# Kernel tuning notes

Measured on AMD Instinct MI355X. Metric: run time of the kernel, lower is better.

The kernel has to match this reference:

```python
import jax, jax.numpy as jnp
import numpy as np

H = 16  # num_heads
D = 1024  # hidden_dim
HD = D // H  # head_dim


def setup_inputs() -> dict:
    key = jax.random.key(0)
    ks = jax.random.split(key, 12)
    B, S = 2, 2048
    x = jax.random.normal(ks[0], (B, S, D), dtype=jnp.float32)
    attention_bias = jax.random.normal(ks[1], (H, S, S), dtype=jnp.float32) * 0.1
    # padding mask: True = masked; last (S - len) positions padded, no all-masked rows
    lengths = jax.random.randint(ks[2], (B,), S // 2, S + 1)
    key_padding_mask = jnp.arange(S)[None, :] >= lengths[:, None]  # [B, S] bool
    s = 1.0 / np.sqrt(D)
    Wq = jax.random.normal(ks[3], (D, D), dtype=jnp.float32) * s
    bq = jnp.zeros((D,), dtype=jnp.float32)
    Wk = jax.random.normal(ks[4], (D, D), dtype=jnp.float32) * s
    bk = jnp.zeros((D,), dtype=jnp.float32)
    Wv = jax.random.normal(ks[5], (D, D), dtype=jnp.float32) * s
    bv = jnp.zeros((D,), dtype=jnp.float32)
    Wo = jax.random.normal(ks[6], (D, D), dtype=jnp.float32) * s
    bo = jnp.zeros((D,), dtype=jnp.float32)
    return {"x": x, "attention_bias": attention_bias, "key_padding_mask": key_padding_mask,
            "Wq": Wq, "bq": bq, "Wk": Wk, "bk": bk, "Wv": Wv, "bv": bv, "Wo": Wo, "bo": bo}


def reference(x, attention_bias, key_padding_mask, Wq, bq, Wk, bk, Wv, bv, Wo, bo):
    B, S, _ = x.shape
    scale = HD ** (-0.5)

    def shape_heads(t):  # [B,S,D] -> [B,H,S,HD]
        return t.reshape(B, S, H, HD).transpose(0, 2, 1, 3)

    q = shape_heads(x @ Wq + bq)
    k = shape_heads(x @ Wk + bk)
    v = shape_heads(x @ Wv + bv)

    attn = jnp.einsum('bhqd,bhkd->bhqk', q, k) * scale  # [B,H,S,S]
    attn = attn + attention_bias[None]
    attn = jnp.where(key_padding_mask[:, None, None, :], -jnp.inf, attn)

    # handle fully-masked rows: zero their logits pre-softmax, zero weights after
    all_masked = jnp.all(key_padding_mask, axis=1)  # [B]
    bad = all_masked[:, None, None, None]
    safe_attn = jnp.where(bad, 0.0, attn)
    weights = jax.nn.softmax(safe_attn, axis=-1)
    weights = jnp.where(bad, 0.0, weights)

    context = jnp.einsum('bhqk,bhkd->bhqd', weights, v)  # [B,H,S,HD]
    context = context.transpose(0, 2, 1, 3).reshape(B, S, D)
    return context @ Wo + bo
```

## Files before the change

kernel.cpp:

```cpp
#include <hip/hip_runtime.h>
#include <hip/hip_bf16.h>
#include <stdint.h>

#define BB 2
#define SS 2048
#define DDIM 1024
#define HH 16
#define HDIM 64

typedef __hip_bfloat16 bf16;
typedef __bf16 bf16x8 __attribute__((ext_vector_type(8)));
typedef float f32x4 __attribute__((ext_vector_type(4)));
typedef short short8 __attribute__((ext_vector_type(8)));
typedef short s16x4 __attribute__((ext_vector_type(4)));

static __device__ __forceinline__ f32x4 mfma16(bf16x8 a, bf16x8 b, f32x4 c) {
  return __builtin_amdgcn_mfma_f32_16x16x32_bf16(a, b, c, 0, 0, 0);
}

static __device__ __forceinline__ void gload_lds16(const void* g, void* l) {
  __builtin_amdgcn_global_load_lds(
      (const __attribute__((address_space(1))) void*)g,
      (__attribute__((address_space(3))) void*)l, 16, 0, 0);
}

__global__ __launch_bounds__(256) void cvt_k(const float* __restrict__ src,
                                             bf16* __restrict__ dst) {
  const int base = (blockIdx.x * 256 + threadIdx.x) * 8;
  float4 a = *reinterpret_cast<const float4*>(src + base);
  float4 b = *reinterpret_cast<const float4*>(src + base + 4);
  union {
    bf16 h[8];
    short8 v;
  } u;
  u.h[0] = __float2bfloat16(a.x);
  u.h[1] = __float2bfloat16(a.y);
  u.h[2] = __float2bfloat16(a.z);
  u.h[3] = __float2bfloat16(a.w);
  u.h[4] = __float2bfloat16(b.x);
  u.h[5] = __float2bfloat16(b.y);
  u.h[6] = __float2bfloat16(b.z);
  u.h[7] = __float2bfloat16(b.w);
  *reinterpret_cast<short8*>(dst + base) = u.v;
}

__global__ __launch_bounds__(256) void transpose_cvt_k(
    const float* __restrict__ src, bf16* __restrict__ dst) {
  __shared__ float tile[64][65];
  const int t = threadIdx.x;
  const int r = t >> 2, c0 = (t & 3) * 16;
  const int bx = blockIdx.x * 64, by = blockIdx.y * 64;
  const float* sp = src + (size_t)(by + r) * DDIM + bx + c0;
#pragma unroll
  for (int j = 0; j < 16; ++j) tile[r][c0 + j] = sp[j];
  __syncthreads();
  bf16* dp = dst + (size_t)(bx + r) * DDIM + by + c0;
#pragma unroll
  for (int j = 0; j < 16; ++j) dp[j] = __float2bfloat16(tile[c0 + j][r]);
}

__global__ __launch_bounds__(64) void mask_pack_k(
    const int* __restrict__ kpm, unsigned long long* __restrict__ mb) {
  const int i = threadIdx.x;
  const int b = i >> 5, c = i & 31;
  unsigned long long bits = 0ull;
  for (int j = 0; j < 64; ++j)
    bits |= (unsigned long long)(kpm[b * SS + c * 64 + j] != 0) << j;
  mb[i] = bits;
}

template <int MODE>
__global__ __launch_bounds__(256, 2) void gemm_bt(
    const bf16* __restrict__ A, const bf16* __restrict__ Bt,
    const float* __restrict__ b0, const float* __restrict__ b1,
    const float* __restrict__ b2, bf16* __restrict__ O0,
    bf16* __restrict__ O1, bf16* __restrict__ O2, float* __restrict__ Of) {
  constexpr int Kd = DDIM;
  __shared__ bf16x8 lA[128 * 8];
  __shared__ bf16x8 lB[128 * 8];
  const int tid = threadIdx.x;
  const int wave = tid >> 6, lane = tid & 63;
  const int l15 = lane & 15, l4 = lane >> 4;
  const int wm = wave >> 1, wn = wave & 1;
  const int m0 = blockIdx.x * 128, n0 = blockIdx.y * 128;
  const f32x4 z = {0.f, 0.f, 0.f, 0.f};
  f32x4 acc[4][4];
#pragma unroll
  for (int i = 0; i < 4; ++i)
#pragma unroll
    for (int j = 0; j < 4; ++j) acc[i][j] = z;

  for (int k0 = 0; k0 < Kd; k0 += 64) {
#pragma unroll
    for (int j = 0; j < 4; ++j) {
      const int slot = j * 256 + tid;
      const int r = slot >> 3, cs = slot & 7;
      const int c = cs ^ (r & 7);
      gload_lds16(A + (size_t)(m0 + r) * Kd + k0 + c * 8,
                  &lA[j * 256 + wave * 64]);
      gload_lds16(Bt + (size_t)(n0 + r) * Kd + k0 + c * 8,
                  &lB[j * 256 + wave * 64]);
    }
    __syncthreads();
    bf16x8 af[2][4], bfr[2][4];
#pragma unroll
    for (int ks = 0; ks < 2; ++ks) {
#pragma unroll
      for (int i = 0; i < 4; ++i) {
        const int ra = wm * 64 + i * 16 + l15;
        af[ks][i] = lA[ra * 8 + ((ks * 4 + l4) ^ (ra & 7))];
        const int rb = wn * 64 + i * 16 + l15;
        bfr[ks][i] = lB[rb * 8 + ((ks * 4 + l4) ^ (rb & 7))];
      }
    }
#pragma unroll
    for (int ks = 0; ks < 2; ++ks)
#pragma unroll
      for (int i = 0; i < 4; ++i)
#pragma unroll
        for (int j = 0; j < 4; ++j)
          acc[i][j] = mfma16(af[ks][i], bfr[ks][j], acc[i][j]);
    __syncthreads();
  }

#pragma unroll
  for (int i = 0; i < 4; ++i) {
    const int m = m0 + wm * 64 + i * 16 + l4 * 4;
#pragma unroll
    for (int j = 0; j < 4; ++j) {
      const int n = n0 + wn * 64 + j * 16 + l15;
      if (MODE == 1) {
        const float bb = b0[n];
#pragma unroll
        for (int r = 0; r < 4; ++r)
          Of[(size_t)(m + r) * DDIM + n] = acc[i][j][r] + bb;
      } else {
        const int sel = n >> 10, nn = n & 1023;
        const int h = nn >> 6, d = nn & 63;
        const float* bp = sel == 0 ? b0 : (sel == 1 ? b1 : b2);
        const float bb = bp[nn];
        const int b = m >> 11, s = m & 2047;
        if (sel == 2) {
          union {
            bf16 h4[4];
            s16x4 v;
          } u;
#pragma unroll
          for (int r = 0; r < 4; ++r)
            u.h4[r] = __float2bfloat16(acc[i][j][r] + bb);
          *reinterpret_cast<s16x4*>(
              &O2[((size_t)(b * HH + h) * HDIM + d) * SS + s]) = u.v;
        } else {
#pragma unroll
          for (int r = 0; r < 4; ++r) {
            const float val = acc[i][j][r] + bb;
            (sel ? O1 : O0)[((size_t)(b * HH + h) * SS + (s + r)) * HDIM + d] =
                __float2bfloat16(val);
          }
        }
      }
    }
  }
}

__global__ __launch_bounds__(256, 2) void attn_k(
    const bf16* __restrict__ Qb, const bf16* __restrict__ Kb,
    const bf16* __restrict__ Vt, const float* __restrict__ bias,
    const unsigned long long* __restrict__ mbits, bf16* __restrict__ ctx) {
  __shared__ bf16x8 lK[2][512];
  __shared__ bf16x8 lV[2][512];
  __shared__ f32x4 lB[2][1024];
  __shared__ unsigned int plP[4 * 512];
  const int tid = threadIdx.x;
  const int wave = tid >> 6, lane = tid & 63;
  const int l15 = lane & 15, l4 = lane >> 4;
  const int bid = blockIdx.x;
  const int qblk = bid & 31, bh = bid >> 5;
  const int b = bh >> 4, h = bh & 15;
  const int q0b = qblk * 64;
  const int q0w = q0b + wave * 16;

  const bf16* Qp = Qb + ((size_t)bh * SS + q0w) * HDIM;
  const bf16* Kp = Kb + (size_t)bh * SS * HDIM;
  const bf16* Vp = Vt + (size_t)bh * HDIM * SS;
  const float* Bb = bias + (size_t)h * SS * SS + (size_t)q0b * SS;
  unsigned int* plw = plP + wave * 512;

  const int rk0 = tid >> 3, ck0 = tid & 7;
  const int rk1 = 32 + rk0, ck1 = ck0;
  const int dk0 = rk0 * 8 + (ck0 ^ (rk0 & 7));
  const int dk1 = rk1 * 8 + (ck1 ^ (rk1 & 7));
  int rbv[4], cbv[4], dbv[4];
#pragma unroll
  for (int i = 0; i < 4; ++i) {
    const int sb = i * 256 + tid;
    rbv[i] = sb >> 4;
    cbv[i] = sb & 15;
    dbv[i] = rbv[i] * 16 + (cbv[i] ^ (rbv[i] & 7));
  }
  const int brow = wave * 16 + l15;

  {
    bf16x8 k0 = *reinterpret_cast<const bf16x8*>(Kp + (size_t)rk0 * HDIM + ck0 * 8);
    bf16x8 k1 = *reinterpret_cast<const bf16x8*>(Kp + (size_t)rk1 * HDIM + ck1 * 8);
    bf16x8 v0 = *reinterpret_cast<const bf16x8*>(Vp + (size_t)rk0 * SS + ck0 * 8);
    bf16x8 v1 = *reinterpret_cast<const bf16x8*>(Vp + (size_t)rk1 * SS + ck1 * 8);
    f32x4 b0 = *reinterpret_cast<const f32x4*>(Bb + (size_t)rbv[0] * SS + cbv[0] * 4);
    f32x4 b1 = *reinterpret_cast<const f32x4*>(Bb + (size_t)rbv[1] * SS + cbv[1] * 4);
    f32x4 b2 = *reinterpret_cast<const f32x4*>(Bb + (size_t)rbv[2] * SS + cbv[2] * 4);
    f32x4 b3 = *reinterpret_cast<const f32x4*>(Bb + (size_t)rbv[3] * SS + cbv[3] * 4);
    lK[0][dk0] = k0;
    lK[0][dk1] = k1;
    lV[0][dk0] = v0;
    lV[0][dk1] = v1;
    lB[0][dbv[0]] = b0;
    lB[0][dbv[1]] = b1;
    lB[0][dbv[2]] = b2;
    lB[0][dbv[3]] = b3;
  }

  bf16x8 qf[2];
#pragma unroll
  for (int ks = 0; ks < 2; ++ks)
    qf[ks] = *reinterpret_cast<const bf16x8*>(Qp + (size_t)l15 * HDIM +
                                              ks * 32 + l4 * 8);
  const f32x4 z = {0.f, 0.f, 0.f, 0.f};
  f32x4 o[4];
#pragma unroll
  for (int dd = 0; dd < 4; ++dd) o[dd] = z;
  float mrow = -1e30f, lrow = 0.f;

  __syncthreads();

  for (int t = 0; t < 32; ++t) {
    const int cur = t & 1;
    const int kbn = (t + 1) * 64;
    const bool pf = t < 31;

    bf16x8 ks0, ks1, vs0, vs1;
    f32x4 bs0, bs1, bs2, bs3;
    if (pf) {
      ks0 = *reinterpret_cast<const bf16x8*>(Kp + (size_t)(kbn + rk0) * HDIM + ck0 * 8);
      ks1 = *reinterpret_cast<const bf16x8*>(Kp + (size_t)(kbn + rk1) * HDIM + ck1 * 8);
      vs0 = *reinterpret_cast<const bf16x8*>(Vp + (size_t)rk0 * SS + kbn + ck0 * 8);
      vs1 = *reinterpret_cast<const bf16x8*>(Vp + (size_t)rk1 * SS + kbn + ck1 * 8);
      bs0 = *reinterpret_cast<const f32x4*>(Bb + (size_t)rbv[0] * SS + kbn + cbv[0] * 4);
      bs1 = *reinterpret_cast<const f32x4*>(Bb + (size_t)rbv[1] * SS + kbn + cbv[1] * 4);
      bs2 = *reinterpret_cast<const f32x4*>(Bb + (size_t)rbv[2] * SS + kbn + cbv[2] * 4);
      bs3 = *reinterpret_cast<const f32x4*>(Bb + (size_t)rbv[3] * SS + kbn + cbv[3] * 4);
    }

    f32x4 sc[4];
#pragma unroll
    for (int jj = 0; jj < 4; ++jj) {
      const int R = jj * 16 + l15;
      bf16x8 kf0 = lK[cur][R * 8 + ((0 + l4) ^ (R & 7))];
      bf16x8 kf1 = lK[cur][R * 8 + ((4 + l4) ^ (R & 7))];
      f32x4 s = mfma16(kf0, qf[0], z);
      s = mfma16(kf1, qf[1], s);
      sc[jj] = s;
    }
    const unsigned long long mb = mbits[(b << 5) + t];
    float v[4][4];
    float bm = -1e30f;
#pragma unroll
    for (int jj = 0; jj < 4; ++jj) {
      const int byte =
          brow * 256 + ((((jj * 4 + l4) ^ (l15 & 7))) * 16);
      const f32x4 b4 = *reinterpret_cast<const f32x4*>(
          reinterpret_cast<const char*>(&lB[cur][0]) + byte);
      const unsigned nib = (unsigned)(mb >> (jj * 16 + l4 * 4)) & 15u;
#pragma unroll
      for (int r = 0; r < 4; ++r) {
        const float a = ((nib >> r) & 1u) ? -1e30f : b4[r];
        v[jj][r] = fmaf(sc[jj][r], 0.125f, a);
        bm = fmaxf(bm, v[jj][r]);
      }
    }
    bm = fmaxf(bm, __shfl_xor(bm, 16));
    bm = fmaxf(bm, __shfl_xor(bm, 32));
    const float mn = fmaxf(mrow, bm);
    const float alpha = __expf(mrow - mn);
    mrow = mn;
    float ps = 0.f;
    float p[4][4];
#pragma unroll
    for (int jj = 0; jj < 4; ++jj)
#pragma unroll
      for (int r = 0; r < 4; ++r) {
        p[jj][r] = __expf(v[jj][r] - mn);
        ps += p[jj][r];
      }
    ps += __shfl_xor(ps, 16);
    ps += __shfl_xor(ps, 32);
    lrow = lrow * alpha + ps;
#pragma unroll
    for (int jj = 0; jj < 4; ++jj)
#pragma unroll
      for (int r0 = 0; r0 < 4; r0 += 2) {
        union {
          bf16 h2[2];
          unsigned int w;
        } u;
        u.h2[0] = __float2bfloat16(p[jj][r0]);
        u.h2[1] = __float2bfloat16(p[jj][r0 + 1]);
        const int byte =
            (l15 * 128 + jj * 32 + l4 * 8 + r0 * 2) ^ ((l15 & 7) << 4);
        plw[byte >> 2] = u.w;
      }
    asm volatile("s_waitcnt lgkmcnt(0)" ::: "memory");
    bf16x8 pfr[2];
#pragma unroll
    for (int ks = 0; ks < 2; ++ks) {
      const int byte = (l15 * 128 + ks * 64 + l4 * 16) ^ ((l15 & 7) << 4);
      pfr[ks] = *reinterpret_cast<const bf16x8*>(
          reinterpret_cast<const char*>(plw) + byte);
    }
    float ar[4];
#pragma unroll
    for (int r = 0; r < 4; ++r) ar[r] = __shfl(alpha, l4 * 4 + r);
#pragma unroll
    for (int dd = 0; dd < 4; ++dd) {
      const int D = dd * 16 + l15;
      bf16x8 vf0 = lV[cur][D * 8 + ((0 + l4) ^ (D & 7))];
      bf16x8 vf1 = lV[cur][D * 8 + ((4 + l4) ^ (D & 7))];
#pragma unroll
      for (int r = 0; r < 4; ++r) o[dd][r] *= ar[r];
      o[dd] = mfma16(pfr[0], vf0, o[dd]);
      o[dd] = mfma16(pfr[1], vf1, o[dd]);
    }

    if (pf) {
      const int nxt = cur ^ 1;
      lK[nxt][dk0] = ks0;
      lK[nxt][dk1] = ks1;
      lV[nxt][dk0] = vs0;
      lV[nxt][dk1] = vs1;
      lB[nxt][dbv[0]] = bs0;
      lB[nxt][dbv[1]] = bs1;
      lB[nxt][dbv[2]] = bs2;
      lB[nxt][dbv[3]] = bs3;
    }
    __syncthreads();
  }

  const float rl = 1.0f / lrow;
  float rlr[4];
#pragma unroll
  for (int r = 0; r < 4; ++r) rlr[r] = __shfl(rl, l4 * 4 + r);
#pragma unroll
  for (int dd = 0; dd < 4; ++dd) {
#pragma unroll
    for (int r = 0; r < 4; ++r) {
      const float val = o[dd][r] * rlr[r];
      const int s = q0w + l4 * 4 + r;
      ctx[((size_t)b * SS + s) * DDIM + h * HDIM + dd * 16 + l15] =
          __float2bfloat16(val);
    }
  }
}

extern "C" void kernel_launch(void* const* d_in, const int* in_sizes, int n_in,
                              void* d_out, int out_size, void* d_ws,
                              size_t ws_size, hipStream_t stream) {
  const float* x = (const float*)d_in[0];
  const float* abias = (const float*)d_in[1];
  const int* kpm = (const int*)d_in[2];
  const float* Wq = (const float*)d_in[3];
  const float* bq = (const float*)d_in[4];
  const float* Wk = (const float*)d_in[5];
  const float* bk = (const float*)d_in[6];
  const float* Wv = (const float*)d_in[7];
  const float* bv = (const float*)d_in[8];
  const float* Wo = (const float*)d_in[9];
  const float* bo = (const float*)d_in[10];
  float* out = (float*)d_out;

  char* ws = (char*)d_ws;
  bf16* xb = (bf16*)ws;
  bf16* Wt = (bf16*)(ws + 8388608);
  bf16* Wot = (bf16*)(ws + 14680064);
  bf16* Qb = (bf16*)(ws + 16777216);
  bf16* Kb = (bf16*)(ws + 25165824);
  bf16* Vtb = (bf16*)(ws + 33554432);
  bf16* ctx = (bf16*)(ws + 41943040);
  unsigned long long* mbits =
      (unsigned long long*)(ws + 50331648);

  dim3 t256(256);
  cvt_k<<<dim3(2048), t256, 0, stream>>>(x, xb);
  transpose_cvt_k<<<dim3(16, 16), t256, 0, stream>>>(Wq, Wt);
  transpose_cvt_k<<<dim3(16, 16), t256, 0, stream>>>(Wk, Wt + 1024 * 1024);
  transpose_cvt_k<<<dim3(16, 16), t256, 0, stream>>>(Wv, Wt + 2 * 1024 * 1024);
  transpose_cvt_k<<<dim3(16, 16), t256, 0, stream>>>(Wo, Wot);
  mask_pack_k<<<dim3(1), dim3(64), 0, stream>>>(kpm, mbits);

  gemm_bt<0><<<dim3(32, 24), t256, 0, stream>>>(xb, Wt, bq, bk, bv, Qb, Kb,
                                                Vtb, nullptr);
  attn_k<<<dim3(1024), t256, 0, stream>>>(Qb, Kb, Vtb, abias, mbits, ctx);
  gemm_bt<1><<<dim3(32, 8), t256, 0, stream>>>(ctx, Wot, bo, nullptr, nullptr,
                                               nullptr, nullptr, nullptr, out);
}
```

Baseline: 212.6 us.

## Load attention bias directly into registers, drop LDS staging, raise occupancy

The bias tile is no longer staged through shared memory. Each lane now loads the bias values it needs straight from global memory into registers, double-buffered by ping-ponging two register sets across an unrolled pair of iterations. This frees 32KB of LDS per block, and launch bounds are raised to allow 4 blocks per CU. The cost is less coalesced per-lane bias loads (16B chunks spread across 16 rows) and more register pressure under the tighter occupancy bound.

After: 286.7 us. +34.8%, slower.

```diff
diff --git a/kernel.cpp b/kernel.cpp
--- a/kernel.cpp
+++ b/kernel.cpp
@@ -163,13 +163,12 @@
   }
 }
 
-__global__ __launch_bounds__(256, 2) void attn_k(
+__global__ __launch_bounds__(256, 4) void attn_k(
     const bf16* __restrict__ Qb, const bf16* __restrict__ Kb,
     const bf16* __restrict__ Vt, const float* __restrict__ bias,
     const unsigned long long* __restrict__ mbits, bf16* __restrict__ ctx) {
   __shared__ bf16x8 lK[2][512];
   __shared__ bf16x8 lV[2][512];
-  __shared__ f32x4 lB[2][1024];
   __shared__ unsigned int plP[4 * 512];
   const int tid = threadIdx.x;
   const int wave = tid >> 6, lane = tid & 63;
@@ -183,41 +182,29 @@
   const bf16* Qp = Qb + ((size_t)bh * SS + q0w) * HDIM;
   const bf16* Kp = Kb + (size_t)bh * SS * HDIM;
   const bf16* Vp = Vt + (size_t)bh * HDIM * SS;
-  const float* Bb = bias + (size_t)h * SS * SS + (size_t)q0b * SS;
+  const float* Bp = bias + (size_t)h * SS * SS + (size_t)(q0w + l15) * SS;
   unsigned int* plw = plP + wave * 512;
 
   const int rk0 = tid >> 3, ck0 = tid & 7;
   const int rk1 = 32 + rk0, ck1 = ck0;
   const int dk0 = rk0 * 8 + (ck0 ^ (rk0 & 7));
   const int dk1 = rk1 * 8 + (ck1 ^ (rk1 & 7));
-  int rbv[4], cbv[4], dbv[4];
-#pragma unroll
-  for (int i = 0; i < 4; ++i) {
-    const int sb = i * 256 + tid;
-    rbv[i] = sb >> 4;
-    cbv[i] = sb & 15;
-    dbv[i] = rbv[i] * 16 + (cbv[i] ^ (rbv[i] & 7));
-  }
-  const int brow = wave * 16 + l15;
 
   {
     bf16x8 k0 = *reinterpret_cast<const bf16x8*>(Kp + (size_t)rk0 * HDIM + ck0 * 8);
     bf16x8 k1 = *reinterpret_cast<const bf16x8*>(Kp + (size_t)rk1 * HDIM + ck1 * 8);
     bf16x8 v0 = *reinterpret_cast<const bf16x8*>(Vp + (size_t)rk0 * SS + ck0 * 8);
     bf16x8 v1 = *reinterpret_cast<const bf16x8*>(Vp + (size_t)rk1 * SS + ck1 * 8);
-    f32x4 b0 = *reinterpret_cast<const f32x4*>(Bb + (size_t)rbv[0] * SS + cbv[0] * 4);
-    f32x4 b1 = *reinterpret_cast<const f32x4*>(Bb + (size_t)rbv[1] * SS + cbv[1] * 4);
-    f32x4 b2 = *reinterpret_cast<const f32x4*>(Bb + (size_t)rbv[2] * SS + cbv[2] * 4);
-    f32x4 b3 = *reinterpret_cast<const f32x4*>(Bb + (size_t)rbv[3] * SS + cbv[3] * 4);
     lK[0][dk0] = k0;
     lK[0][dk1] = k1;
     lV[0][dk0] = v0;
     lV[0][dk1] = v1;
-    lB[0][dbv[0]] = b0;
-    lB[0][dbv[1]] = b1;
-    lB[0][dbv[2]] = b2;
-    lB[0][dbv[3]] = b3;
-  }
+  }
+  f32x4 bA0 = *reinterpret_cast<const f32x4*>(Bp + 0 * 16 + l4 * 4);
+  f32x4 bA1 = *reinterpret_cast<const f32x4*>(Bp + 1 * 16 + l4 * 4);
+  f32x4 bA2 = *reinterpret_cast<const f32x4*>(Bp + 2 * 16 + l4 * 4);
+  f32x4 bA3 = *reinterpret_cast<const f32x4*>(Bp + 3 * 16 + l4 * 4);
+  f32x4 bB0, bB1, bB2, bB3;
 
   bf16x8 qf[2];
 #pragma unroll
@@ -232,22 +219,22 @@
 
   __syncthreads();
 
-  for (int t = 0; t < 32; ++t) {
+  auto step = [&](int t, f32x4 bc0, f32x4 bc1, f32x4 bc2, f32x4 bc3,
+                  f32x4& bn0, f32x4& bn1, f32x4& bn2, f32x4& bn3) {
     const int cur = t & 1;
     const int kbn = (t + 1) * 64;
     const bool pf = t < 31;
 
     bf16x8 ks0, ks1, vs0, vs1;
-    f32x4 bs0, bs1, bs2, bs3;
     if (pf) {
       ks0 = *reinterpret_cast<const bf16x8*>(Kp + (size_t)(kbn + rk0) * HDIM + ck0 * 8);
       ks1 = *reinterpret_cast<const bf16x8*>(Kp + (size_t)(kbn + rk1) * HDIM + ck1 * 8);
       vs0 = *reinterpret_cast<const bf16x8*>(Vp + (size_t)rk0 * SS + kbn + ck0 * 8);
       vs1 = *reinterpret_cast<const bf16x8*>(Vp + (size_t)rk1 * SS + kbn + ck1 * 8);
-      bs0 = *reinterpret_cast<const f32x4*>(Bb + (size_t)rbv[0] * SS + kbn + cbv[0] * 4);
-      bs1 = *reinterpret_cast<const f32x4*>(Bb + (size_t)rbv[1] * SS + kbn + cbv[1] * 4);
-      bs2 = *reinterpret_cast<const f32x4*>(Bb + (size_t)rbv[2] * SS + kbn + cbv[2] * 4);
-      bs3 = *reinterpret_cast<const f32x4*>(Bb + (size_t)rbv[3] * SS + kbn + cbv[3] * 4);
+      bn0 = *reinterpret_cast<const f32x4*>(Bp + kbn + 0 * 16 + l4 * 4);
+      bn1 = *reinterpret_cast<const f32x4*>(Bp + kbn + 1 * 16 + l4 * 4);
+      bn2 = *reinterpret_cast<const f32x4*>(Bp + kbn + 2 * 16 + l4 * 4);
+      bn3 = *reinterpret_cast<const f32x4*>(Bp + kbn + 3 * 16 + l4 * 4);
     }
 
     f32x4 sc[4];
@@ -260,19 +247,16 @@
       s = mfma16(kf1, qf[1], s);
       sc[jj] = s;
     }
+    const f32x4 bcs[4] = {bc0, bc1, bc2, bc3};
     const unsigned long long mb = mbits[(b << 5) + t];
     float v[4][4];
     float bm = -1e30f;
 #pragma unroll
     for (int jj = 0; jj < 4; ++jj) {
-      const int byte =
-          brow * 256 + ((((jj * 4 + l4) ^ (l15 & 7))) * 16);
-      const f32x4 b4 = *reinterpret_cast<const f32x4*>(
-          reinterpret_cast<const char*>(&lB[cur][0]) + byte);
       const unsigned nib = (unsigned)(mb >> (jj * 16 + l4 * 4)) & 15u;
 #pragma unroll
       for (int r = 0; r < 4; ++r) {
-        const float a = ((nib >> r) & 1u) ? -1e30f : b4[r];
+        const float a = ((nib >> r) & 1u) ? -1e30f : bcs[jj][r];
         v[jj][r] = fmaf(sc[jj][r], 0.125f, a);
         bm = fmaxf(bm, v[jj][r]);
       }
@@ -336,12 +320,13 @@
       lK[nxt][dk1] = ks1;
       lV[nxt][dk0] = vs0;
       lV[nxt][dk1] = vs1;
-      lB[nxt][dbv[0]] = bs0;
-      lB[nxt][dbv[1]] = bs1;
-      lB[nxt][dbv[2]] = bs2;
-      lB[nxt][dbv[3]] = bs3;
     }
     __syncthreads();
+  };
+
+  for (int t2 = 0; t2 < 16; ++t2) {
+    step(t2 * 2, bA0, bA1, bA2, bA3, bB0, bB1, bB2, bB3);
+    step(t2 * 2 + 1, bB0, bB1, bB2, bB3, bA0, bA1, bA2, bA3);
   }
 
   const float rl = 1.0f / lrow;
```
